# Optimization experiments

Measured on AMD Instinct MI355X. Metric: run time of the kernel, lower is better.

Reference implementation:

```python
import jax, jax.numpy as jnp
import numpy as np

C = 256
CQK = C // 8  # 32

def setup_inputs() -> dict:
    key = jax.random.key(0)
    ks = jax.random.split(key, 9)
    B, H, W = 4, 64, 64
    s = 0.02
    return {
        "x": jax.random.normal(ks[0], (B, C, W, H), jnp.float32),
        "y": jax.random.normal(ks[1], (B, C, W, H), jnp.float32),
        "Wq": jax.random.normal(ks[2], (CQK, C), jnp.float32) * s,
        "bq": jax.random.normal(ks[3], (CQK,), jnp.float32) * s,
        "Wk": jax.random.normal(ks[4], (CQK, C), jnp.float32) * s,
        "bk": jax.random.normal(ks[5], (CQK,), jnp.float32) * s,
        "Wv": jax.random.normal(ks[6], (C, C), jnp.float32) * s,
        "bv": jax.random.normal(ks[7], (C,), jnp.float32) * s,
        "gamma": jnp.zeros((1,), jnp.float32) + 0.1,  # nonzero so output depends on attention
    }

def reference(x, y, Wq, bq, Wk, bk, Wv, bv, gamma):
    B, Cc, Wd, Hd = x.shape
    N = Wd * Hd
    xf = x.reshape(B, Cc, N)  # [B,C,N]
    yf = y.reshape(B, Cc, N)
    # 1x1 convs == channel matmuls
    q = jnp.einsum('dc,bcn->bnd', Wq, xf) + bq  # [B,N,CQK]
    k = jnp.einsum('dc,bcn->bdn', Wk, yf) + bk[None, :, None]  # [B,CQK,N]
    v = jnp.einsum('ec,bcn->ben', Wv, yf) + bv[None, :, None]  # [B,C,N]
    energy = jnp.einsum('bnd,bdm->bnm', q, k)  # [B,N,N]
    attn = jax.nn.softmax(energy, axis=-1)
    out = jnp.einsum('bem,bnm->ben', v, attn)  # [B,C,N]
    out = out.reshape(B, Cc, Wd, Hd)
    return gamma * out + x
```

## Files before the change

### kernel.cpp

```cpp
#include <hip/hip_runtime.h>
#include <hip/hip_bf16.h>
#include <stdint.h>

#define B_   4
#define C_   256
#define CQK_ 32
#define N_   4096

typedef float f32x4  __attribute__((ext_vector_type(4)));
typedef short bf16x8 __attribute__((ext_vector_type(8)));
typedef unsigned uint4v __attribute__((ext_vector_type(4)));

__device__ __forceinline__ unsigned short f2bf(float f) {
    unsigned u = __builtin_bit_cast(unsigned, f);
    u += 0x7FFFu + ((u >> 16) & 1u);
    return (unsigned short)(u >> 16);
}
__device__ __forceinline__ unsigned pack2(float a, float b) {
    return (unsigned)f2bf(a) | ((unsigned)f2bf(b) << 16);
}

__device__ __forceinline__ size_t vfrag_off(int b, int e, int m) {
    return ((((size_t)b * 128 + (m >> 5)) * 16 + (e >> 4)) * 64
            + (size_t)((m >> 3) & 3) * 16 + (e & 15)) * 8 + (m & 7);
}

__global__ __launch_bounds__(256) void transpose_kernel(
        const float* __restrict__ x, const float* __restrict__ y,
        const float* __restrict__ Wq, const float* __restrict__ Wk,
        const float* __restrict__ Wv,
        unsigned short* __restrict__ xb, unsigned short* __restrict__ yb,
        unsigned short* __restrict__ Wqb, unsigned short* __restrict__ Wkb,
        unsigned short* __restrict__ Wvb) {
    const int bid = blockIdx.x, tid = threadIdx.x;
    if (bid < 512) {
        __shared__ char lds[64 * 528];
        const bool isx = bid < 256;
        const int slab = bid & 255;
        const int b  = slab >> 6;
        const int n0 = (slab & 63) * 64;
        const float* __restrict__ src = isx ? x : y;
        unsigned short* __restrict__ dst = isx ? xb : yb;
        const int l = tid & 63, wv = tid >> 6;
        const float* sp = src + (size_t)(b * C_) * N_ + n0 + l;
#pragma unroll
        for (int i = 0; i < 64; i += 2) {
            const int c = wv * 64 + i;
            const float v0 = sp[(size_t)c * N_];
            const float v1 = sp[(size_t)(c + 1) * N_];
            *(unsigned*)(lds + l * 528 + c * 2) = pack2(v0, v1);
        }
        __syncthreads();
        const int n = tid >> 5, chunk = tid & 31;
#pragma unroll
        for (int j = 0; j < 8; ++j) {
            const int nn = n + j * 8;
            const uint4v v = *(const uint4v*)(lds + nn * 528 + chunk * 16);
            *(uint4v*)((char*)(dst + ((size_t)b * N_ + n0 + nn) * C_) + chunk * 16) = v;
        }
    } else {
        for (int p = (bid - 512) * 256 + tid; p < 40960; p += 64 * 256) {
            const float* s; unsigned short* d; int off;
            if (p < 4096)      { s = Wq; d = Wqb; off = p; }
            else if (p < 8192) { s = Wk; d = Wkb; off = p - 4096; }
            else               { s = Wv; d = Wvb; off = p - 8192; }
            *(unsigned*)(d + off * 2) = pack2(s[off * 2], s[off * 2 + 1]);
        }
    }
}

__global__ __launch_bounds__(256) void proj_gemm(
        const unsigned short* __restrict__ xb, const unsigned short* __restrict__ yb,
        const unsigned short* __restrict__ Wqb, const unsigned short* __restrict__ Wkb,
        const unsigned short* __restrict__ Wvb,
        const float* __restrict__ bq, const float* __restrict__ bk,
        const float* __restrict__ bv,
        unsigned short* __restrict__ qf, unsigned short* __restrict__ kf,
        unsigned short* __restrict__ vf) {
    const int tid = threadIdx.x, w = tid >> 6, l = tid & 63;
    const int lr = l & 15, lg = l >> 4;
    const int gid = blockIdx.x;
    const int b  = (gid >> 1) & 3;
    const int n0 = ((((gid >> 3) << 1) | (gid & 1))) * 64;

    f32x4 accV[4][4];
    f32x4 accQ[4];
#pragma unroll
    for (int e = 0; e < 4; ++e)
#pragma unroll
        for (int m = 0; m < 4; ++m) accV[e][m] = (f32x4){0.f, 0.f, 0.f, 0.f};
#pragma unroll
    for (int m = 0; m < 4; ++m) accQ[m] = (f32x4){0.f, 0.f, 0.f, 0.f};

    const unsigned short* __restrict__ Wqk = (w < 2) ? Wqb : Wkb;
    const int d0 = (w & 1) * 16;

#pragma unroll
    for (int ks = 0; ks < 8; ++ks) {
        const int c0 = ks * 32 + lg * 8;
        bf16x8 aY[4], aS[4];
#pragma unroll
        for (int mb = 0; mb < 4; ++mb)
            aY[mb] = *(const bf16x8*)(yb + ((size_t)b * N_ + n0 + mb * 16 + lr) * C_ + c0);
        if (w < 2) {
#pragma unroll
            for (int mb = 0; mb < 4; ++mb)
                aS[mb] = *(const bf16x8*)(xb + ((size_t)b * N_ + n0 + mb * 16 + lr) * C_ + c0);
        } else {
#pragma unroll
            for (int mb = 0; mb < 4; ++mb) aS[mb] = aY[mb];
        }
        bf16x8 bV[4];
#pragma unroll
        for (int eb = 0; eb < 4; ++eb)
            bV[eb] = *(const bf16x8*)(Wvb + (size_t)(w * 64 + eb * 16 + lr) * C_ + c0);
        const bf16x8 bQ = *(const bf16x8*)(Wqk + (size_t)(d0 + lr) * C_ + c0);
#pragma unroll
        for (int eb = 0; eb < 4; ++eb)
#pragma unroll
            for (int mb = 0; mb < 4; ++mb)
                accV[eb][mb] = __builtin_amdgcn_mfma_f32_16x16x32_bf16(
                    aY[mb], bV[eb], accV[eb][mb], 0, 0, 0);
#pragma unroll
        for (int mb = 0; mb < 4; ++mb)
            accQ[mb] = __builtin_amdgcn_mfma_f32_16x16x32_bf16(aS[mb], bQ, accQ[mb], 0, 0, 0);
    }

#pragma unroll
    for (int eb = 0; eb < 4; ++eb) {
        const int e = w * 64 + eb * 16 + lr;
        const float bve = bv[e];
#pragma unroll
        for (int mb = 0; mb < 4; ++mb) {
            const size_t off = vfrag_off(b, e, n0 + mb * 16 + lg * 4);
            unsigned* p = (unsigned*)(vf + off);
            p[0] = pack2(accV[eb][mb][0] + bve, accV[eb][mb][1] + bve);
            p[1] = pack2(accV[eb][mb][2] + bve, accV[eb][mb][3] + bve);
        }
    }
    const float bqv = ((w < 2) ? bq : bk)[d0 + lr];
    unsigned short* __restrict__ dqk = (w < 2) ? qf : kf;
#pragma unroll
    for (int mb = 0; mb < 4; ++mb)
#pragma unroll
        for (int r = 0; r < 4; ++r) {
            const int n = n0 + mb * 16 + lg * 4 + r;
            dqk[((size_t)b * N_ + n) * CQK_ + d0 + lr] = f2bf(accQ[mb][r] + bqv);
        }
}

__global__ __launch_bounds__(512, 2) void attn_kernel(
        const unsigned short* __restrict__ qf, const unsigned short* __restrict__ kf,
        const unsigned short* __restrict__ vf, const float* __restrict__ x,
        const float* __restrict__ gamma, float* __restrict__ out) {
    __shared__ char plds[2][64 * 272];
    __shared__ float cLs[8][64];
    __shared__ float cLt[64];
    const int tid = threadIdx.x, w = tid >> 6, l = tid & 63;
    const int lr = l & 15, lg = l >> 4;
    const int gid = blockIdx.x;
    const int b  = (gid >> 1) & 3;
    const int q0 = ((((gid >> 3) << 1) | (gid & 1))) * 64;

    bf16x8 qfr[4];
#pragma unroll
    for (int qblk = 0; qblk < 4; ++qblk)
        qfr[qblk] = *(const bf16x8*)(
            qf + ((size_t)b * N_ + q0 + qblk * 16 + lr) * CQK_ + lg * 8);

    f32x4 acc[4][2];
#pragma unroll
    for (int i = 0; i < 4; ++i) { acc[i][0] = (f32x4){0,0,0,0}; acc[i][1] = (f32x4){0,0,0,0}; }
    float Lacc[4] = {0.f, 0.f, 0.f, 0.f};

    const unsigned short* kbase = kf + ((size_t)b * N_ + w * 16 + lr) * CQK_ + lg * 8;

#define PREFETCH(KT, KFR, VB)                                                  \
    {                                                                          \
        const int t_ = (KT) & 31;                                              \
        KFR = *(const bf16x8*)(kbase + (size_t)t_ * 128 * CQK_);               \
        _Pragma("unroll")                                                      \
        for (int ks_ = 0; ks_ < 4; ++ks_)                                      \
            _Pragma("unroll")                                                  \
            for (int ebi_ = 0; ebi_ < 2; ++ebi_)                               \
                VB[ebi_][ks_] = *(const bf16x8*)(                              \
                    vf + ((((size_t)(b * 128 + t_ * 4 + ks_)) * 16             \
                           + w * 2 + ebi_) * 64 + l) * 8);                     \
    }

#define TILE_BODY(PW, KFR, VB)                                                 \
    {                                                                          \
        f32x4 e4_[4];                                                          \
        _Pragma("unroll")                                                      \
        for (int qblk = 0; qblk < 4; ++qblk)                                   \
            e4_[qblk] = __builtin_amdgcn_mfma_f32_16x16x32_bf16(               \
                KFR, qfr[qblk], (f32x4){0.f, 0.f, 0.f, 0.f}, 0, 0, 0);         \
        const int m2_ = w * 16 + lg * 4;                                       \
        _Pragma("unroll")                                                      \
        for (int qblk = 0; qblk < 4; ++qblk) {                                 \
            const float p0 = __expf(e4_[qblk][0]);                             \
            const float p1 = __expf(e4_[qblk][1]);                             \
            const float p2 = __expf(e4_[qblk][2]);                             \
            const float p3 = __expf(e4_[qblk][3]);                             \
            Lacc[qblk] += (p0 + p1) + (p2 + p3);                               \
            unsigned u0, u1;                                                   \
            asm("v_cvt_pk_bf16_f32 %0, %1, %2" : "=v"(u0) : "v"(p0), "v"(p1)); \
            asm("v_cvt_pk_bf16_f32 %0, %1, %2" : "=v"(u1) : "v"(p2), "v"(p3)); \
            const int q_ = qblk * 16 + lr;                                     \
            const int byte_ = q_ * 272 + ((m2_ >> 3) << 4) + (m2_ & 7) * 2;    \
            *(unsigned long long*)((PW) + byte_) =                             \
                (unsigned long long)u0 | ((unsigned long long)u1 << 32);       \
        }                                                                      \
        asm volatile("s_waitcnt lgkmcnt(0)" ::: "memory");                     \
        __builtin_amdgcn_s_barrier();                                          \
        asm volatile("" ::: "memory");                                         \
        __builtin_amdgcn_s_setprio(1);                                         \
        _Pragma("unroll")                                                      \
        for (int ks_ = 0; ks_ < 4; ++ks_)                                      \
            _Pragma("unroll")                                                  \
            for (int qblk = 0; qblk < 4; ++qblk) {                             \
                const int q_ = qblk * 16 + lr;                                 \
                const bf16x8 pa_ = *(const bf16x8*)(                           \
                    (PW) + q_ * 272 + ((ks_ * 4 + lg) << 4));                  \
                acc[qblk][0] = __builtin_amdgcn_mfma_f32_16x16x32_bf16(        \
                    pa_, VB[0][ks_], acc[qblk][0], 0, 0, 0);                   \
                acc[qblk][1] = __builtin_amdgcn_mfma_f32_16x16x32_bf16(        \
                    pa_, VB[1][ks_], acc[qblk][1], 0, 0, 0);                   \
            }                                                                  \
        __builtin_amdgcn_s_setprio(0);                                         \
    }

    bf16x8 kA, kB;
    bf16x8 vA[2][4], vB[2][4];
    PREFETCH(0, kA, vA);
    PREFETCH(1, kB, vB);

    for (int kt = 0; kt < 32; kt += 2) {
        TILE_BODY(plds[0], kA, vA);
        PREFETCH(kt + 2, kA, vA);
        TILE_BODY(plds[1], kB, vB);
        PREFETCH(kt + 3, kB, vB);
    }
#undef PREFETCH
#undef TILE_BODY

#pragma unroll
    for (int qblk = 0; qblk < 4; ++qblk) {
        Lacc[qblk] += __shfl_xor(Lacc[qblk], 16);
        Lacc[qblk] += __shfl_xor(Lacc[qblk], 32);
    }
    if (l < 16) {
#pragma unroll
        for (int qblk = 0; qblk < 4; ++qblk) cLs[w][qblk * 16 + lr] = Lacc[qblk];
    }
    __syncthreads();
    if (tid < 64) {
        float s = 0.f;
#pragma unroll
        for (int w2 = 0; w2 < 8; ++w2) s += cLs[w2][tid];
        cLt[tid] = 1.0f / s;
    }
    __syncthreads();

    const float g = gamma[0];
#pragma unroll
    for (int qblk = 0; qblk < 4; ++qblk) {
        float rI[4];
#pragma unroll
        for (int r = 0; r < 4; ++r) rI[r] = cLt[qblk * 16 + lg * 4 + r];
        const int nb = q0 + qblk * 16 + lg * 4;
#pragma unroll
        for (int ebi = 0; ebi < 2; ++ebi) {
            const int e = (w * 2 + ebi) * 16 + lr;
            const size_t idx = ((size_t)b * C_ + e) * N_ + nb;
            const f32x4 xv = *(const f32x4*)(x + idx);
            f32x4 ov;
#pragma unroll
            for (int r = 0; r < 4; ++r)
                ov[r] = g * acc[qblk][ebi][r] * rI[r] + xv[r];
            *(f32x4*)(out + idx) = ov;
        }
    }
}

extern "C" void kernel_launch(void* const* d_in, const int* in_sizes, int n_in,
                              void* d_out, int out_size, void* d_ws, size_t ws_size,
                              hipStream_t stream) {
    (void)in_sizes; (void)n_in; (void)out_size; (void)ws_size;
    const float* x     = (const float*)d_in[0];
    const float* y     = (const float*)d_in[1];
    const float* Wq    = (const float*)d_in[2];
    const float* bq    = (const float*)d_in[3];
    const float* Wk    = (const float*)d_in[4];
    const float* bk    = (const float*)d_in[5];
    const float* Wv    = (const float*)d_in[6];
    const float* bv    = (const float*)d_in[7];
    const float* gamma = (const float*)d_in[8];
    float* out = (float*)d_out;

    unsigned short* qf  = (unsigned short*)d_ws;
    unsigned short* kf  = qf + (size_t)B_ * N_ * CQK_;
    unsigned short* vf  = kf + (size_t)B_ * N_ * CQK_;
    unsigned short* Wqb = vf + (size_t)B_ * N_ * C_;
    unsigned short* Wkb = Wqb + CQK_ * C_;
    unsigned short* Wvb = Wkb + CQK_ * C_;

    unsigned short* xb = (unsigned short*)d_out;
    unsigned short* yb = xb + (size_t)B_ * N_ * C_;

    transpose_kernel<<<dim3(576), 256, 0, stream>>>(x, y, Wq, Wk, Wv, xb, yb, Wqb, Wkb, Wvb);
    proj_gemm<<<dim3(256), 256, 0, stream>>>(xb, yb, Wqb, Wkb, Wvb, bq, bk, bv, qf, kf, vf);
    attn_kernel<<<dim3(256), 512, 0, stream>>>(qf, kf, vf, x, gamma, out);
}
```

Baseline: 77.37 us.

## Double key tile width to 256 and load V fragments inline instead of prefetching

Each iteration now processes 256 keys instead of 128, with each wave computing two QK halves, so there are half as many barriers. The shared P buffer row stride grows from 272 to 528 bytes. V fragments are no longer prefetched into registers a tile ahead; they are loaded from global memory right before each PV MFMA, which lowers register pressure. In exchange, V load latency is exposed inside the MFMA loop, and the larger LDS footprint could limit occupancy.

New measurement: 101.7 us. 31.5% more time.

```diff
diff --git a/kernel.cpp b/kernel.cpp
--- a/kernel.cpp
+++ b/kernel.cpp
@@ -153,7 +153,7 @@
         const unsigned short* __restrict__ qf, const unsigned short* __restrict__ kf,
         const unsigned short* __restrict__ vf, const float* __restrict__ x,
         const float* __restrict__ gamma, float* __restrict__ out) {
-    __shared__ char plds[2][64 * 272];
+    __shared__ char plds[2][64 * 528];
     __shared__ float cLs[8][64];
     __shared__ float cLt[64];
     const int tid = threadIdx.x, w = tid >> 6, l = tid & 63;
@@ -173,29 +173,23 @@
     for (int i = 0; i < 4; ++i) { acc[i][0] = (f32x4){0,0,0,0}; acc[i][1] = (f32x4){0,0,0,0}; }
     float Lacc[4] = {0.f, 0.f, 0.f, 0.f};
 
-    const unsigned short* kbase = kf + ((size_t)b * N_ + w * 16 + lr) * CQK_ + lg * 8;
-
-#define PREFETCH(KT, KFR, VB)                                                  \
+    const unsigned short* kbase = kf + ((size_t)b * N_ + lr) * CQK_ + lg * 8;
+
+#define PREF_K(T, K)                                                           \
     {                                                                          \
-        const int t_ = (KT) & 31;                                              \
-        KFR = *(const bf16x8*)(kbase + (size_t)t_ * 128 * CQK_);               \
-        _Pragma("unroll")                                                      \
-        for (int ks_ = 0; ks_ < 4; ++ks_)                                      \
-            _Pragma("unroll")                                                  \
-            for (int ebi_ = 0; ebi_ < 2; ++ebi_)                               \
-                VB[ebi_][ks_] = *(const bf16x8*)(                              \
-                    vf + ((((size_t)(b * 128 + t_ * 4 + ks_)) * 16             \
-                           + w * 2 + ebi_) * 64 + l) * 8);                     \
-    }
-
-#define TILE_BODY(PW, KFR, VB)                                                 \
+        const int t_ = (T) & 15;                                               \
+        K[0] = *(const bf16x8*)(kbase + (size_t)(t_ * 256 + w * 16) * CQK_);   \
+        K[1] = *(const bf16x8*)(kbase + (size_t)(t_ * 256 + (w + 8) * 16) * CQK_); \
+    }
+
+#define HALF_QK(K, H, PW)                                                      \
     {                                                                          \
         f32x4 e4_[4];                                                          \
         _Pragma("unroll")                                                      \
         for (int qblk = 0; qblk < 4; ++qblk)                                   \
             e4_[qblk] = __builtin_amdgcn_mfma_f32_16x16x32_bf16(               \
-                KFR, qfr[qblk], (f32x4){0.f, 0.f, 0.f, 0.f}, 0, 0, 0);         \
-        const int m2_ = w * 16 + lg * 4;                                       \
+                K[H], qfr[qblk], (f32x4){0.f, 0.f, 0.f, 0.f}, 0, 0, 0);        \
+        const int mh_ = (w + (H) * 8) * 16 + lg * 4;                           \
         _Pragma("unroll")                                                      \
         for (int qblk = 0; qblk < 4; ++qblk) {                                 \
             const float p0 = __expf(e4_[qblk][0]);                             \
@@ -207,42 +201,54 @@
             asm("v_cvt_pk_bf16_f32 %0, %1, %2" : "=v"(u0) : "v"(p0), "v"(p1)); \
             asm("v_cvt_pk_bf16_f32 %0, %1, %2" : "=v"(u1) : "v"(p2), "v"(p3)); \
             const int q_ = qblk * 16 + lr;                                     \
-            const int byte_ = q_ * 272 + ((m2_ >> 3) << 4) + (m2_ & 7) * 2;    \
+            const int byte_ = q_ * 528 + ((mh_ >> 3) << 4) + (mh_ & 7) * 2;    \
             *(unsigned long long*)((PW) + byte_) =                             \
                 (unsigned long long)u0 | ((unsigned long long)u1 << 32);       \
         }                                                                      \
+    }
+
+#define BODY(T, K, KN)                                                         \
+    {                                                                          \
+        char* pw_ = plds[(T) & 1];                                             \
+        HALF_QK(K, 0, pw_);                                                    \
+        HALF_QK(K, 1, pw_);                                                    \
         asm volatile("s_waitcnt lgkmcnt(0)" ::: "memory");                     \
         __builtin_amdgcn_s_barrier();                                          \
         asm volatile("" ::: "memory");                                         \
+        PREF_K((T) + 2, K);               \
         __builtin_amdgcn_s_setprio(1);                                         \
         _Pragma("unroll")                                                      \
-        for (int ks_ = 0; ks_ < 4; ++ks_)                                      \
+        for (int ks_ = 0; ks_ < 8; ++ks_) {                                    \
+            const unsigned short* vp_ =                                        \
+                vf + ((size_t)(b * 128 + (T) * 8 + ks_) * 16) * 512;           \
             _Pragma("unroll")                                                  \
             for (int qblk = 0; qblk < 4; ++qblk) {                             \
                 const int q_ = qblk * 16 + lr;                                 \
                 const bf16x8 pa_ = *(const bf16x8*)(                           \
-                    (PW) + q_ * 272 + ((ks_ * 4 + lg) << 4));                  \
-                acc[qblk][0] = __builtin_amdgcn_mfma_f32_16x16x32_bf16(        \
-                    pa_, VB[0][ks_], acc[qblk][0], 0, 0, 0);                   \
-                acc[qblk][1] = __builtin_amdgcn_mfma_f32_16x16x32_bf16(        \
-                    pa_, VB[1][ks_], acc[qblk][1], 0, 0, 0);                   \
+                    pw_ + q_ * 528 + ((ks_ * 4 + lg) << 4));                   \
+                _Pragma("unroll")                                              \
+                for (int ebi_ = 0; ebi_ < 2; ++ebi_) {                         \
+                    const bf16x8 vbf_ = *(const bf16x8*)(                      \
+                        vp_ + ((w * 2 + ebi_) * 64 + l) * 8);                  \
+                    acc[qblk][ebi_] = __builtin_amdgcn_mfma_f32_16x16x32_bf16( \
+                        pa_, vbf_, acc[qblk][ebi_], 0, 0, 0);                  \
+                }                                                              \
             }                                                                  \
+        }                                                                      \
         __builtin_amdgcn_s_setprio(0);                                         \
     }
 
-    bf16x8 kA, kB;
-    bf16x8 vA[2][4], vB[2][4];
-    PREFETCH(0, kA, vA);
-    PREFETCH(1, kB, vB);
-
-    for (int kt = 0; kt < 32; kt += 2) {
-        TILE_BODY(plds[0], kA, vA);
-        PREFETCH(kt + 2, kA, vA);
-        TILE_BODY(plds[1], kB, vB);
-        PREFETCH(kt + 3, kB, vB);
-    }
-#undef PREFETCH
-#undef TILE_BODY
+    bf16x8 kA[2], kB[2];
+    PREF_K(0, kA);
+    PREF_K(1, kB);
+
+    for (int t = 0; t < 16; t += 2) {
+        BODY(t, kA, kAn);
+        BODY(t + 1, kB, kBn);
+    }
+#undef PREF_K
+#undef HALF_QK
+#undef BODY
 
 #pragma unroll
     for (int qblk = 0; qblk < 4; ++qblk) {
```

## Split PV matmul across warps by key slice with LDS cross-warp reduction

Applied to the files above, without the earlier changes.

Each warp now covers all 128 channels of its channel half for one 32-key slice of every tile, instead of 32 channels over all keys. The goal is to cut repeated LDS reads of the P fragments: each warp reads 4 instead of 16 per tile. Partial outputs are then summed across the four key-slice warps through a new 64KB LDS buffer over three synchronised rounds. The K prefetch moves to just after the barrier, and V is prefetched one tile ahead into a single buffer. The accumulator grows fourfold, so register pressure, LDS use and the extra reduction barriers may cut occupancy or cause spills.

Result: faster. 75.82 us (-2.0%).

```diff
diff --git a/kernel.cpp b/kernel.cpp
--- a/kernel.cpp
+++ b/kernel.cpp
@@ -154,6 +154,7 @@
         const unsigned short* __restrict__ vf, const float* __restrict__ x,
         const float* __restrict__ gamma, float* __restrict__ out) {
     __shared__ char plds[2][64 * 272];
+    __shared__ float oslab[2][64][128];
     __shared__ float cLs[8][64];
     __shared__ float cLt[64];
     const int tid = threadIdx.x, w = tid >> 6, l = tid & 63;
@@ -161,6 +162,7 @@
     const int gid = blockIdx.x;
     const int b  = (gid >> 1) & 3;
     const int q0 = ((((gid >> 3) << 1) | (gid & 1))) * 64;
+    const int eh = w >> 2, ksw = w & 3;
 
     bf16x8 qfr[4];
 #pragma unroll
@@ -168,33 +170,36 @@
         qfr[qblk] = *(const bf16x8*)(
             qf + ((size_t)b * N_ + q0 + qblk * 16 + lr) * CQK_ + lg * 8);
 
-    f32x4 acc[4][2];
-#pragma unroll
-    for (int i = 0; i < 4; ++i) { acc[i][0] = (f32x4){0,0,0,0}; acc[i][1] = (f32x4){0,0,0,0}; }
+    f32x4 acc[4][8];
+#pragma unroll
+    for (int i = 0; i < 4; ++i)
+#pragma unroll
+        for (int j = 0; j < 8; ++j) acc[i][j] = (f32x4){0.f, 0.f, 0.f, 0.f};
     float Lacc[4] = {0.f, 0.f, 0.f, 0.f};
 
     const unsigned short* kbase = kf + ((size_t)b * N_ + w * 16 + lr) * CQK_ + lg * 8;
 
-#define PREFETCH(KT, KFR, VB)                                                  \
+#define PREF_K(T, K)                                                           \
+    K = *(const bf16x8*)(kbase + (size_t)(((T) & 31) * 128) * CQK_);
+
+#define PREF_V(T)                                                              \
     {                                                                          \
-        const int t_ = (KT) & 31;                                              \
-        KFR = *(const bf16x8*)(kbase + (size_t)t_ * 128 * CQK_);               \
+        const int t_ = (T) & 31;                                               \
         _Pragma("unroll")                                                      \
-        for (int ks_ = 0; ks_ < 4; ++ks_)                                      \
-            _Pragma("unroll")                                                  \
-            for (int ebi_ = 0; ebi_ < 2; ++ebi_)                               \
-                VB[ebi_][ks_] = *(const bf16x8*)(                              \
-                    vf + ((((size_t)(b * 128 + t_ * 4 + ks_)) * 16             \
-                           + w * 2 + ebi_) * 64 + l) * 8);                     \
-    }
-
-#define TILE_BODY(PW, KFR, VB)                                                 \
+        for (int ebi_ = 0; ebi_ < 8; ++ebi_)                                   \
+            vV[ebi_] = *(const bf16x8*)(                                       \
+                vf + ((size_t)((b * 128 + t_ * 4 + ksw) * 16 + eh * 8 + ebi_)) \
+                         * 512 + l * 8);                                       \
+    }
+
+#define BODY(T, K)                                                             \
     {                                                                          \
         f32x4 e4_[4];                                                          \
         _Pragma("unroll")                                                      \
         for (int qblk = 0; qblk < 4; ++qblk)                                   \
             e4_[qblk] = __builtin_amdgcn_mfma_f32_16x16x32_bf16(               \
-                KFR, qfr[qblk], (f32x4){0.f, 0.f, 0.f, 0.f}, 0, 0, 0);         \
+                K, qfr[qblk], (f32x4){0.f, 0.f, 0.f, 0.f}, 0, 0, 0);           \
+        char* pw_ = plds[(T) & 1];                                             \
         const int m2_ = w * 16 + lg * 4;                                       \
         _Pragma("unroll")                                                      \
         for (int qblk = 0; qblk < 4; ++qblk) {                                 \
@@ -208,41 +213,40 @@
             asm("v_cvt_pk_bf16_f32 %0, %1, %2" : "=v"(u1) : "v"(p2), "v"(p3)); \
             const int q_ = qblk * 16 + lr;                                     \
             const int byte_ = q_ * 272 + ((m2_ >> 3) << 4) + (m2_ & 7) * 2;    \
-            *(unsigned long long*)((PW) + byte_) =                             \
+            *(unsigned long long*)(pw_ + byte_) =                              \
                 (unsigned long long)u0 | ((unsigned long long)u1 << 32);       \
         }                                                                      \
         asm volatile("s_waitcnt lgkmcnt(0)" ::: "memory");                     \
         __builtin_amdgcn_s_barrier();                                          \
         asm volatile("" ::: "memory");                                         \
+        PREF_K((T) + 2, K);                                                    \
         __builtin_amdgcn_s_setprio(1);                                         \
         _Pragma("unroll")                                                      \
-        for (int ks_ = 0; ks_ < 4; ++ks_)                                      \
+        for (int qblk = 0; qblk < 4; ++qblk) {                                 \
+            const int q_ = qblk * 16 + lr;                                     \
+            const bf16x8 pa_ = *(const bf16x8*)(                               \
+                pw_ + q_ * 272 + ((ksw * 4 + lg) << 4));                       \
             _Pragma("unroll")                                                  \
-            for (int qblk = 0; qblk < 4; ++qblk) {                             \
-                const int q_ = qblk * 16 + lr;                                 \
-                const bf16x8 pa_ = *(const bf16x8*)(                           \
-                    (PW) + q_ * 272 + ((ks_ * 4 + lg) << 4));                  \
-                acc[qblk][0] = __builtin_amdgcn_mfma_f32_16x16x32_bf16(        \
-                    pa_, VB[0][ks_], acc[qblk][0], 0, 0, 0);                   \
-                acc[qblk][1] = __builtin_amdgcn_mfma_f32_16x16x32_bf16(        \
-                    pa_, VB[1][ks_], acc[qblk][1], 0, 0, 0);                   \
-            }                                                                  \
+            for (int ebi_ = 0; ebi_ < 8; ++ebi_)                               \
+                acc[qblk][ebi_] = __builtin_amdgcn_mfma_f32_16x16x32_bf16(     \
+                    pa_, vV[ebi_], acc[qblk][ebi_], 0, 0, 0);                  \
+        }                                                                      \
         __builtin_amdgcn_s_setprio(0);                                         \
-    }
-
-    bf16x8 kA, kB;
-    bf16x8 vA[2][4], vB[2][4];
-    PREFETCH(0, kA, vA);
-    PREFETCH(1, kB, vB);
+        PREF_V((T) + 1);                  \
+    }
+
+    bf16x8 kA, kB, vV[8];
+    PREF_K(0, kA);
+    PREF_K(1, kB);
+    PREF_V(0);
 
     for (int kt = 0; kt < 32; kt += 2) {
-        TILE_BODY(plds[0], kA, vA);
-        PREFETCH(kt + 2, kA, vA);
-        TILE_BODY(plds[1], kB, vB);
-        PREFETCH(kt + 3, kB, vB);
-    }
-#undef PREFETCH
-#undef TILE_BODY
+        BODY(kt, kA);
+        BODY(kt + 1, kB);
+    }
+#undef PREF_K
+#undef PREF_V
+#undef BODY
 
 #pragma unroll
     for (int qblk = 0; qblk < 4; ++qblk) {
@@ -259,6 +263,40 @@
 #pragma unroll
         for (int w2 = 0; w2 < 8; ++w2) s += cLs[w2][tid];
         cLt[tid] = 1.0f / s;
+    }
+    __syncthreads();
+
+#pragma unroll
+    for (int round = 3; round > 0; --round) {
+        if (ksw == round) {
+#pragma unroll
+            for (int qblk = 0; qblk < 4; ++qblk)
+#pragma unroll
+                for (int ebi = 0; ebi < 8; ++ebi)
+#pragma unroll
+                    for (int r = 0; r < 4; ++r)
+                        oslab[eh][qblk * 16 + lg * 4 + r][ebi * 16 + lr] = acc[qblk][ebi][r];
+        }
+        __syncthreads();
+        if (ksw == round - 1) {
+#pragma unroll
+            for (int qblk = 0; qblk < 4; ++qblk)
+#pragma unroll
+                for (int ebi = 0; ebi < 8; ++ebi)
+#pragma unroll
+                    for (int r = 0; r < 4; ++r)
+                        acc[qblk][ebi][r] += oslab[eh][qblk * 16 + lg * 4 + r][ebi * 16 + lr];
+        }
+        __syncthreads();
+    }
+    if (ksw == 0) {
+#pragma unroll
+        for (int qblk = 0; qblk < 4; ++qblk)
+#pragma unroll
+            for (int ebi = 0; ebi < 8; ++ebi)
+#pragma unroll
+                for (int r = 0; r < 4; ++r)
+                    oslab[eh][qblk * 16 + lg * 4 + r][ebi * 16 + lr] = acc[qblk][ebi][r];
     }
     __syncthreads();
 
@@ -276,8 +314,10 @@
             const f32x4 xv = *(const f32x4*)(x + idx);
             f32x4 ov;
 #pragma unroll
-            for (int r = 0; r < 4; ++r)
-                ov[r] = g * acc[qblk][ebi][r] * rI[r] + xv[r];
+            for (int r = 0; r < 4; ++r) {
+                const float val = oslab[e >> 7][qblk * 16 + lg * 4 + r][e & 127];
+                ov[r] = g * val * rI[r] + xv[r];
+            }
             *(f32x4*)(out + idx) = ov;
         }
     }
```
